# Optimization experiments

Hardware: AMD Instinct MI355X
Metric: run time of the kernel (lower is better)

Reference implementation:

```python
import jax, jax.numpy as jnp
import numpy as np

B, T, D, H = 2, 2048, 1024, 16
DK = D // H
SCALE = 1.0 / float(np.sqrt(DK))


def setup_inputs() -> dict:
    key0 = jax.random.key(0)
    ks = jax.random.split(key0, 12)
    std = 0.02
    inp = {
        "query": jax.random.normal(ks[0], (B, T, D), jnp.float32),
        "key": jax.random.normal(ks[1], (B, T, D), jnp.float32),
        "value": jax.random.normal(ks[2], (B, T, D), jnp.float32),
        # weights stored torch-style: out = x @ W.T + b, W is [D, D]
        "Wq": jax.random.normal(ks[3], (D, D), jnp.float32) * std,
        "bq": jnp.zeros((D,), jnp.float32),
        "Wk": jax.random.normal(ks[4], (D, D), jnp.float32) * std,
        "bk": jnp.zeros((D,), jnp.float32),
        "Wv": jax.random.normal(ks[5], (D, D), jnp.float32) * std,
        "bv": jnp.zeros((D,), jnp.float32),
        "Wo": jax.random.normal(ks[6], (D, D), jnp.float32) * std,
        "bo": jnp.zeros((D,), jnp.float32),
        # causal mask: True = masked out (matches masked_fill semantics)
        "attn_mask": jnp.triu(jnp.ones((T, T), jnp.bool_), k=1),
        # no padding (all False) to keep every softmax row valid
        "key_padding_mask": jnp.zeros((B, T), jnp.bool_),
    }
    return inp


def reference(query, key, value, Wq, bq, Wk, bk, Wv, bv, Wo, bo,
              attn_mask, key_padding_mask):
    Bq, Tq, _ = query.shape
    Tk = key.shape[1]
    # QKV projections, split into heads: [B, T, H, DK]
    q = (query @ Wq.T + bq).reshape(Bq, Tq, H, DK)
    k = (key @ Wk.T + bk).reshape(Bq, Tk, H, DK)
    v = (value @ Wv.T + bv).reshape(Bq, Tk, H, DK)
    # scaled dot-product scores: [B, H, Tq, Tk]
    scores = jnp.einsum("bqhd,bkhd->bhqk", q, k) * jnp.float32(SCALE)
    neg_inf = jnp.float32(-jnp.inf)
    scores = jnp.where(attn_mask[None, None, :, :], neg_inf, scores)
    scores = jnp.where(key_padding_mask[:, None, None, :], neg_inf, scores)
    attn = jax.nn.softmax(scores, axis=-1)
    out = jnp.einsum("bhqk,bkhd->bqhd", attn, v).reshape(Bq, Tq, D)
    return out @ Wo.T + bo
```

## Files before the change

### kernel.cpp

```cpp
#include <hip/hip_runtime.h>
#include <hip/hip_bf16.h>
#include <stdint.h>

#define B_   2
#define T_   2048
#define D_   1024
#define H_   16
#define DK_  64
#define KL2_ 0.18033688f

typedef __attribute__((ext_vector_type(8))) short   short8;
typedef __attribute__((ext_vector_type(4))) float   floatx4;
typedef unsigned short ushort_t;
typedef unsigned int   uint_t;

__device__ __forceinline__ ushort_t f32_to_bf16(float f) {
    union { float f; unsigned int u; } v; v.f = f;
    unsigned int r = v.u + 0x7fffu + ((v.u >> 16) & 1u);
    return (ushort_t)(r >> 16);
}

__device__ __forceinline__ uint_t pk_bf16(float lo, float hi) {
    uint_t ulo = __builtin_bit_cast(uint_t, lo) + 0x8000u;
    uint_t uhi = __builtin_bit_cast(uint_t, hi) + 0x8000u;
    return __builtin_amdgcn_perm(uhi, ulo, 0x07060302);
}

__device__ __forceinline__ void async_copy16(const ushort_t* g, ushort_t* l) {
    typedef const unsigned int __attribute__((address_space(1)))* gp_t;
    typedef       unsigned int __attribute__((address_space(3)))* lp_t;
    __builtin_amdgcn_global_load_lds((gp_t)(uintptr_t)g, (lp_t)(uintptr_t)l, 16, 0, 0);
}

__global__ __launch_bounds__(256) void cast_all_kernel(
    const float* __restrict__ q, const float* __restrict__ k, const float* __restrict__ v,
    const float* __restrict__ wq, const float* __restrict__ wk,
    const float* __restrict__ wv, const float* __restrict__ wo,
    ushort_t* __restrict__ oq, ushort_t* __restrict__ ok, ushort_t* __restrict__ ov,
    ushort_t* __restrict__ owq, ushort_t* __restrict__ owk,
    ushort_t* __restrict__ owv, ushort_t* __restrict__ owo)
{
    const int NTD4 = (B_ * T_ * D_) / 4;
    const int NW4  = (D_ * D_) / 4;
    int i = blockIdx.x * 256 + threadIdx.x;
    const float* s; ushort_t* d; int off;
    if (i < NTD4)              { s = q; d = oq; off = i; }
    else if (i < 2 * NTD4)     { s = k; d = ok; off = i - NTD4; }
    else if (i < 3 * NTD4)     { s = v; d = ov; off = i - 2 * NTD4; }
    else {
        int w = i - 3 * NTD4;
        int seg = w / NW4;  off = w - seg * NW4;
        s = (seg == 0) ? wq : (seg == 1) ? wk : (seg == 2) ? wv : wo;
        d = (seg == 0) ? owq : (seg == 1) ? owk : (seg == 2) ? owv : owo;
    }
    float4 x = ((const float4*)s)[off];
    ushort4 o;
    o.x = f32_to_bf16(x.x); o.y = f32_to_bf16(x.y);
    o.z = f32_to_bf16(x.z); o.w = f32_to_bf16(x.w);
    ((ushort4*)d)[off] = o;
}

#define BM 128
#define BK 32

template<int MODE, int NI>
__device__ __forceinline__ void gemm_bt_device(
    const ushort_t* __restrict__ A, const ushort_t* __restrict__ W,
    const float* __restrict__ bias, void* __restrict__ outp,
    int m0, int n0, ushort_t* sm, float oscale)
{
    const int tid  = threadIdx.x;
    const int lane = tid & 63;
    const int wv   = tid >> 6;
    const int wm   = (wv >> 1) * 64;
    const int wn   = (wv & 1) * (NI * 16);
    const int cl   = lane & 15;
    const int qd   = lane >> 4;
    const int sw4  = (cl >> 1) & 3;

    floatx4 acc[4][NI];
    const floatx4 z4 = {0.f, 0.f, 0.f, 0.f};
    #pragma unroll
    for (int mi = 0; mi < 4; ++mi)
        #pragma unroll
        for (int ni = 0; ni < NI; ++ni) acc[mi][ni] = z4;

    const int r0 = tid >> 2;
    const int cg = (tid & 3) ^ ((r0 >> 1) & 3);
    const ushort_t* Ag0 = A + (size_t)(m0 + r0) * 1024 + cg * 8;
    const ushort_t* Ag1 = A + (size_t)(m0 + 64 + r0) * 1024 + cg * 8;
    const ushort_t* Wg0 = W + (size_t)(n0 + r0) * 1024 + cg * 8;
    const ushort_t* Wg1 = W + (size_t)(n0 + 64 + r0) * 1024 + cg * 8;
    ushort_t* As0 = sm + tid * 8;
    ushort_t* As1 = sm + 2048 + tid * 8;
    ushort_t* Bs0 = sm + 4096 + tid * 8;
    ushort_t* Bs1 = sm + 6144 + tid * 8;

    for (int k0 = 0; k0 < 1024; k0 += BK) {
        async_copy16(Ag0 + k0, As0);
        async_copy16(Ag1 + k0, As1);
        async_copy16(Wg0 + k0, Bs0);
        if (NI == 4) async_copy16(Wg1 + k0, Bs1);
        __syncthreads();

        short8 af[4], bfr[NI];
        #pragma unroll
        for (int mi = 0; mi < 4; ++mi)
            af[mi] = *(const short8*)(sm + (wm + mi * 16 + cl) * 32 + (qd ^ sw4) * 8);
        #pragma unroll
        for (int ni = 0; ni < NI; ++ni)
            bfr[ni] = *(const short8*)(sm + 4096 + (wn + ni * 16 + cl) * 32 + (qd ^ sw4) * 8);

        #pragma unroll
        for (int mi = 0; mi < 4; ++mi)
            #pragma unroll
            for (int ni = 0; ni < NI; ++ni)
                acc[mi][ni] = __builtin_amdgcn_mfma_f32_16x16x32_bf16(
                    af[mi], bfr[ni], acc[mi][ni], 0, 0, 0);
        __syncthreads();
    }

    #pragma unroll
    for (int mi = 0; mi < 4; ++mi) {
        #pragma unroll
        for (int ni = 0; ni < NI; ++ni) {
            const int n = n0 + wn + ni * 16 + cl;
            const float bn = bias[n];
            if (MODE == 0) {
                float* out = (float*)outp;
                #pragma unroll
                for (int r = 0; r < 4; ++r) {
                    const int m = m0 + wm + mi * 16 + qd * 4 + r;
                    out[(size_t)m * D_ + n] = acc[mi][ni][r] + bn;
                }
            } else if (MODE == 1) {
                ushort_t* out = (ushort_t*)outp;
                const int h = n >> 6, dk = n & 63;
                #pragma unroll
                for (int r = 0; r < 4; ++r) {
                    const int m = m0 + wm + mi * 16 + qd * 4 + r;
                    const int b = m >> 11, t = m & (T_ - 1);
                    out[(((size_t)(b * H_ + h)) * T_ + t) * DK_ + dk] =
                        f32_to_bf16((acc[mi][ni][r] + bn) * oscale);
                }
            } else {
                ushort_t* out = (ushort_t*)outp;
                const int h = n >> 6, dk = n & 63;
                const int mb = m0 + wm + mi * 16 + qd * 4;
                const int b = mb >> 11, t0 = mb & (T_ - 1);
                const int tsw = (t0 & ~60) | ((t0 & 48) >> 2) | ((t0 & 12) << 2);
                ushort4 o;
                o.x = f32_to_bf16(acc[mi][ni][0] + bn);
                o.y = f32_to_bf16(acc[mi][ni][1] + bn);
                o.z = f32_to_bf16(acc[mi][ni][2] + bn);
                o.w = f32_to_bf16(acc[mi][ni][3] + bn);
                *(ushort4*)(out + (((size_t)(b * H_ + h)) * DK_ + dk) * T_ + tsw) = o;
            }
        }
    }
}

__global__ __launch_bounds__(256) void gemm_o_kernel(
    const ushort_t* __restrict__ A, const ushort_t* __restrict__ W,
    const float* __restrict__ bias, float* __restrict__ out)
{
    __shared__ __align__(16) ushort_t sm[8192];
    gemm_bt_device<0, 2>(A, W, bias, out, blockIdx.x * BM, blockIdx.y * 64, sm, 1.0f);
}


__device__ __forceinline__ void ldA4(short8 (&af)[4][2], const ushort_t* base, int coff) {
    #pragma unroll
    for (int mi = 0; mi < 4; ++mi) {
        af[mi][0] = *(const short8*)(base + mi * 1024 + coff);
        af[mi][1] = *(const short8*)(base + mi * 1024 + (coff ^ 32));
    }
}
__device__ __forceinline__ void ldB2(short8 (&bf)[2][2], const ushort_t* base, int coff) {
    #pragma unroll
    for (int ni = 0; ni < 2; ++ni) {
        bf[ni][0] = *(const short8*)(base + ni * 1024 + coff);
        bf[ni][1] = *(const short8*)(base + ni * 1024 + (coff ^ 32));
    }
}

template<int MQ, int NQ>
__device__ __forceinline__ void quad16(floatx4 (&acc)[8][4],
                                       const short8 (&af)[4][2],
                                       const short8 (&bf)[2][2])
{
    __builtin_amdgcn_s_setprio(1);
    #pragma unroll
    for (int mi = 0; mi < 4; ++mi)
        #pragma unroll
        for (int ni = 0; ni < 2; ++ni) {
            acc[MQ * 4 + mi][NQ * 2 + ni] = __builtin_amdgcn_mfma_f32_16x16x32_bf16(
                af[mi][0], bf[ni][0], acc[MQ * 4 + mi][NQ * 2 + ni], 0, 0, 0);
            acc[MQ * 4 + mi][NQ * 2 + ni] = __builtin_amdgcn_mfma_f32_16x16x32_bf16(
                af[mi][1], bf[ni][1], acc[MQ * 4 + mi][NQ * 2 + ni], 0, 0, 0);
        }
    __builtin_amdgcn_s_setprio(0);
}

__global__ void __launch_bounds__(512, 2) gemm_qkv8_kernel(
    const ushort_t* __restrict__ Xq, const ushort_t* __restrict__ Xk, const ushort_t* __restrict__ Xv,
    const ushort_t* __restrict__ Wqw, const ushort_t* __restrict__ Wkw, const ushort_t* __restrict__ Wvw,
    const float* __restrict__ bq, const float* __restrict__ bk, const float* __restrict__ bv,
    ushort_t* __restrict__ Qo, ushort_t* __restrict__ Ko, ushort_t* __restrict__ Vto)
{
    extern __shared__ __align__(16) ushort_t sm[];

    const int bid    = blockIdx.x;
    const int gid    = (bid & 7) * 24 + (bid >> 3);
    const int m_tile = gid / 12;
    const int n_tile = gid - m_tile * 12;
    const int m0     = m_tile * 256;
    const int seg    = n_tile >> 2;
    const int n0     = (n_tile & 3) * 256;

    const ushort_t* A    = (seg == 0) ? Xq  : (seg == 1) ? Xk  : Xv;
    const ushort_t* W    = (seg == 0) ? Wqw : (seg == 1) ? Wkw : Wvw;
    const float*    bias = (seg == 0) ? bq  : (seg == 1) ? bk  : bv;

    const int tid  = threadIdx.x;
    const int lane = tid & 63;
    const int wv   = tid >> 6;
    const int wm   = wv >> 2;
    const int wn   = wv & 3;
    const int cl   = lane & 15;
    const int qd   = lane >> 4;
    const int swz  = cl & 7;
    const int coff = (qd ^ swz) * 8;

    const int r0 = tid >> 3;
    const int c0 = (tid & 7) ^ (r0 & 7);
    const ushort_t* gA = A + (size_t)(m0 + r0) * 1024 + c0 * 8;
    const ushort_t* gB = W + (size_t)(n0 + r0) * 1024 + c0 * 8;
    ushort_t* lbase = sm + tid * 8;

    auto stage = [&](int t, int op, int h) {
        if (t >= 16) return;
        const ushort_t* g = (op ? gB : gA) + (size_t)h * 131072 + (size_t)t * 64;
        ushort_t* l = lbase + (size_t)((t & 1) * 4 + op * 2 + h) * 8192;
        async_copy16(g, l);
        async_copy16(g + 65536, l + 4096);
    };

    const ushort_t* A0 = sm + (0 * 4 + 0 * 2 + wm) * 8192 + cl * 64;
    const ushort_t* A1 = A0 + 4 * 8192;
    const ushort_t* B0 = sm + (0 * 4 + 1 * 2 + (wn >> 1)) * 8192 + (wn & 1) * 4096 + cl * 64;
    const ushort_t* B1 = B0 + 4 * 8192;

    floatx4 acc[8][4];
    const floatx4 z4 = {0.f, 0.f, 0.f, 0.f};
    #pragma unroll
    for (int i = 0; i < 8; ++i)
        #pragma unroll
        for (int j = 0; j < 4; ++j) acc[i][j] = z4;

    stage(0, 0, 0); stage(0, 0, 1); stage(0, 1, 0); stage(0, 1, 1);
    stage(1, 1, 0); stage(1, 1, 1);
    asm volatile("s_waitcnt vmcnt(4)" ::: "memory");
    __builtin_amdgcn_s_barrier();

    short8 af[4][2], bf0[2][2], bf1[2][2];

    #pragma unroll 1
    for (int it = 0; it < 7; ++it) {
        const int u = 2 * it, v = u + 1;
        ldA4(af, A0, coff); ldB2(bf0, B0, coff);
        stage(v, 0, 0);
        __builtin_amdgcn_s_barrier();
        quad16<0, 0>(acc, af, bf0);
        __builtin_amdgcn_s_barrier();
        ldB2(bf1, B0 + 2048, coff);
        stage(v, 0, 1);
        __builtin_amdgcn_s_barrier();
        quad16<0, 1>(acc, af, bf1);
        __builtin_amdgcn_s_barrier();
        ldA4(af, A0 + 4096, coff);
        stage(u + 2, 1, 0);
        __builtin_amdgcn_s_barrier();
        quad16<1, 1>(acc, af, bf1);
        __builtin_amdgcn_s_barrier();
        stage(u + 2, 1, 1);
        asm volatile("s_waitcnt vmcnt(4)" ::: "memory");
        __builtin_amdgcn_s_barrier();
        quad16<1, 0>(acc, af, bf0);
        __builtin_amdgcn_s_barrier();
        ldA4(af, A1, coff); ldB2(bf0, B1, coff);
        stage(u + 2, 0, 0);
        __builtin_amdgcn_s_barrier();
        quad16<0, 0>(acc, af, bf0);
        __builtin_amdgcn_s_barrier();
        ldB2(bf1, B1 + 2048, coff);
        stage(u + 2, 0, 1);
        __builtin_amdgcn_s_barrier();
        quad16<0, 1>(acc, af, bf1);
        __builtin_amdgcn_s_barrier();
        ldA4(af, A1 + 4096, coff);
        stage(v + 2, 1, 0);
        __builtin_amdgcn_s_barrier();
        quad16<1, 1>(acc, af, bf1);
        __builtin_amdgcn_s_barrier();
        stage(v + 2, 1, 1);
        asm volatile("s_waitcnt vmcnt(4)" ::: "memory");
        __builtin_amdgcn_s_barrier();
        quad16<1, 0>(acc, af, bf0);
        __builtin_amdgcn_s_barrier();
    }

    ldA4(af, A0, coff); ldB2(bf0, B0, coff);
    stage(15, 0, 0);
    __builtin_amdgcn_s_barrier();
    quad16<0, 0>(acc, af, bf0);
    __builtin_amdgcn_s_barrier();
    ldB2(bf1, B0 + 2048, coff);
    stage(15, 0, 1);
    __builtin_amdgcn_s_barrier();
    quad16<0, 1>(acc, af, bf1);
    __builtin_amdgcn_s_barrier();
    ldA4(af, A0 + 4096, coff);
    __builtin_amdgcn_s_barrier();
    quad16<1, 1>(acc, af, bf1);
    __builtin_amdgcn_s_barrier();
    asm volatile("s_waitcnt vmcnt(0)" ::: "memory");
    __builtin_amdgcn_s_barrier();
    quad16<1, 0>(acc, af, bf0);
    __builtin_amdgcn_s_barrier();
    ldA4(af, A1, coff); ldB2(bf0, B1, coff);
    __builtin_amdgcn_s_barrier();
    quad16<0, 0>(acc, af, bf0);
    __builtin_amdgcn_s_barrier();
    ldB2(bf1, B1 + 2048, coff);
    __builtin_amdgcn_s_barrier();
    quad16<0, 1>(acc, af, bf1);
    __builtin_amdgcn_s_barrier();
    ldA4(af, A1 + 4096, coff);
    __builtin_amdgcn_s_barrier();
    quad16<1, 1>(acc, af, bf1);
    __builtin_amdgcn_s_barrier();
    quad16<1, 0>(acc, af, bf0);

    float bn[4];
    #pragma unroll
    for (int nf = 0; nf < 4; ++nf)
        bn[nf] = bias[n0 + wn * 64 + nf * 16 + cl];

    if (seg < 2) {
        ushort_t* out = (seg == 0) ? Qo : Ko;
        const float oscale = (seg == 0) ? KL2_ : 1.0f;
        #pragma unroll
        for (int mf = 0; mf < 8; ++mf) {
            #pragma unroll
            for (int nf = 0; nf < 4; ++nf) {
                const int n = n0 + wn * 64 + nf * 16 + cl;
                const int h = n >> 6, dk = n & 63;
                #pragma unroll
                for (int r = 0; r < 4; ++r) {
                    const int m = m0 + wm * 128 + mf * 16 + qd * 4 + r;
                    const int b = m >> 11, t = m & (T_ - 1);
                    out[(((size_t)(b * H_ + h)) * T_ + t) * DK_ + dk] =
                        f32_to_bf16((acc[mf][nf][r] + bn[nf]) * oscale);
                }
            }
        }
    } else {
        #pragma unroll
        for (int mf = 0; mf < 8; ++mf) {
            #pragma unroll
            for (int nf = 0; nf < 4; ++nf) {
                const int n = n0 + wn * 64 + nf * 16 + cl;
                const int h = n >> 6, dk = n & 63;
                const int mb = m0 + wm * 128 + mf * 16 + qd * 4;
                const int b = mb >> 11, t0 = mb & (T_ - 1);
                const int tsw = (t0 & ~60) | ((t0 & 48) >> 2) | ((t0 & 12) << 2);
                ushort4 o;
                o.x = f32_to_bf16(acc[mf][nf][0] + bn[nf]);
                o.y = f32_to_bf16(acc[mf][nf][1] + bn[nf]);
                o.z = f32_to_bf16(acc[mf][nf][2] + bn[nf]);
                o.w = f32_to_bf16(acc[mf][nf][3] + bn[nf]);
                *(ushort4*)(Vto + (((size_t)(b * H_ + h)) * DK_ + dk) * T_ + tsw) = o;
            }
        }
    }
}

__global__ __launch_bounds__(256, 2) void attn_kernel(
    const ushort_t* __restrict__ Q, const ushort_t* __restrict__ K,
    const ushort_t* __restrict__ Vs, ushort_t* __restrict__ O)
{
    __shared__ __align__(16) ushort_t sm[32768];
    const int tid  = threadIdx.x;
    const int lane = tid & 63;
    const int wv   = tid >> 6;
    const int cl   = lane & 15;
    const int qd   = lane >> 4;
    const int swz  = cl & 7;
    const int h = blockIdx.x & (H_ - 1), b = blockIdx.x >> 4;
    const int p   = blockIdx.y;
    const int btA = 31 - p;

    const ushort_t* Qh = Q  + ((size_t)(b * H_ + h) * T_) * DK_;
    const ushort_t* Kh = K  + ((size_t)(b * H_ + h) * T_) * DK_;
    const ushort_t* Vh = Vs + ((size_t)(b * H_ + h) * DK_) * T_;

    const int sr  = tid >> 3;
    const int sc  = tid & 7;
    const int scg = sc ^ (sr & 7);

    auto stage_step = [&](int s) {
        const int kbase = ((s <= btA) ? s : (s - btA - 1)) << 6;
        ushort_t* Kb = sm + (s & 3) * 8192;
        ushort_t* Vb = Kb + 4096;
        #pragma unroll
        for (int rr = 0; rr < 2; ++rr) {
            const int r = rr * 32 + sr;
            async_copy16(Kh + (size_t)(kbase + r) * DK_ + scg * 8, Kb + r * 64 + sc * 8);
            async_copy16(Vh + (size_t)r * T_ + kbase + scg * 8,    Vb + r * 64 + sc * 8);
        }
    };

    int qw = btA * 64 + wv * 16;
    short8 qf0 = *(const short8*)(Qh + (size_t)(qw + cl) * DK_ + qd * 8);
    short8 qf1 = *(const short8*)(Qh + (size_t)(qw + cl) * DK_ + 32 + qd * 8);

    stage_step(0);
    stage_step(1);

    const floatx4 z4 = {0.f, 0.f, 0.f, 0.f};
    floatx4 oaccT[4] = {z4, z4, z4, z4};
    float l_ = 0.f;

    auto flush = [&](int q0w) {
        float l = l_;
        l += __shfl_xor(l, 16, 64);
        l += __shfl_xor(l, 32, 64);
        const float inv = 1.0f / l;
        ushort_t* Ob = O + ((size_t)(b * T_ + q0w + cl)) * D_ + h * DK_ + qd * 4;
        #pragma unroll
        for (int dt = 0; dt < 4; ++dt) {
            ushort4 o;
            o.x = f32_to_bf16(oaccT[dt][0] * inv);
            o.y = f32_to_bf16(oaccT[dt][1] * inv);
            o.z = f32_to_bf16(oaccT[dt][2] * inv);
            o.w = f32_to_bf16(oaccT[dt][3] * inv);
            *(ushort4*)(Ob + dt * 16) = o;
        }
    };

    auto compute_step = [&](int s) {
        const bool inA  = (s <= btA);
        const int kbase = (inA ? s : (s - btA - 1)) << 6;
        const bool diag = inA ? (s == btA) : (s == 32);
        ushort_t* cb = sm + (s & 3) * 8192;
        short8 kb[4][2];
        #pragma unroll
        for (int m = 0; m < 4; ++m)
            #pragma unroll
            for (int i = 0; i < 2; ++i)
                kb[m][i] = *(const short8*)(cb + (m * 16 + cl) * 64 + ((i * 4 + qd) ^ swz) * 8);
        floatx4 sacc[4] = {z4, z4, z4, z4};
        #pragma unroll
        for (int i = 0; i < 2; ++i)
            #pragma unroll
            for (int m = 0; m < 4; ++m)
                sacc[m] = __builtin_amdgcn_mfma_f32_16x16x32_bf16(
                    kb[m][i], (i ? qf1 : qf0), sacc[m], 0, 0, 0);
        const int qabs = qw + cl;
        float pr[4][4];
        if (diag) {
            #pragma unroll
            for (int c = 0; c < 4; ++c)
                #pragma unroll
                for (int r = 0; r < 4; ++r) {
                    const bool keep = (kbase + c * 16 + qd * 4 + r) <= qabs;
                    const float e = __builtin_amdgcn_exp2f(sacc[c][r]);
                    pr[c][r] = keep ? e : 0.f;
                    l_ += pr[c][r];
                }
        } else {
            #pragma unroll
            for (int c = 0; c < 4; ++c)
                #pragma unroll
                for (int r = 0; r < 4; ++r) {
                    pr[c][r] = __builtin_amdgcn_exp2f(sacc[c][r]);
                    l_ += pr[c][r];
                }
        }
        short8 va2[4][2];
        #pragma unroll
        for (int dt = 0; dt < 4; ++dt)
            #pragma unroll
            for (int h2 = 0; h2 < 2; ++h2)
                va2[dt][h2] = *(const short8*)(cb + 4096 + (dt * 16 + cl) * 64 +
                                               ((qd * 2 + h2) ^ swz) * 8);
        #pragma unroll
        for (int cp = 0; cp < 2; ++cp) {
            union { uint_t u[4]; short8 v; } pb;
            pb.u[0] = pk_bf16(pr[cp * 2][0],     pr[cp * 2][1]);
            pb.u[1] = pk_bf16(pr[cp * 2][2],     pr[cp * 2][3]);
            pb.u[2] = pk_bf16(pr[cp * 2 + 1][0], pr[cp * 2 + 1][1]);
            pb.u[3] = pk_bf16(pr[cp * 2 + 1][2], pr[cp * 2 + 1][3]);
            #pragma unroll
            for (int dt = 0; dt < 4; ++dt)
                oaccT[dt] = __builtin_amdgcn_mfma_f32_16x16x32_bf16(
                    va2[dt][cp], pb.v, oaccT[dt], 0, 0, 0);
        }
        if (s == btA) {
            flush(qw);
            #pragma unroll
            for (int dt = 0; dt < 4; ++dt) oaccT[dt] = z4;
            l_ = 0.f;
            qw = p * 64 + wv * 16;
            qf0 = *(const short8*)(Qh + (size_t)(qw + cl) * DK_ + qd * 8);
            qf1 = *(const short8*)(Qh + (size_t)(qw + cl) * DK_ + 32 + qd * 8);
        }
    };

    for (int g = 0; g < 17; ++g) {
        const int s0 = g * 2;
        __syncthreads();
        if (s0 + 2 <= 32) stage_step(s0 + 2);
        if (s0 + 3 <= 32) stage_step(s0 + 3);
        compute_step(s0);
        if (s0 + 1 <= 32) compute_step(s0 + 1);
    }
    flush(qw);
}

extern "C" void kernel_launch(void* const* d_in, const int* in_sizes, int n_in,
                              void* d_out, int out_size, void* d_ws, size_t ws_size,
                              hipStream_t stream)
{
    const float* q_in = (const float*)d_in[0];
    const float* k_in = (const float*)d_in[1];
    const float* v_in = (const float*)d_in[2];
    const float* Wq   = (const float*)d_in[3];
    const float* bq   = (const float*)d_in[4];
    const float* Wk   = (const float*)d_in[5];
    const float* bk   = (const float*)d_in[6];
    const float* Wv   = (const float*)d_in[7];
    const float* bv   = (const float*)d_in[8];
    const float* Wo   = (const float*)d_in[9];
    const float* bo   = (const float*)d_in[10];
    float* out = (float*)d_out;

    const size_t NTD = (size_t)B_ * T_ * D_;
    const size_t NW  = (size_t)D_ * D_;
    ushort_t* ws  = (ushort_t*)d_ws;
    ushort_t* Xq  = ws;
    ushort_t* Xk  = Xq + NTD;
    ushort_t* Xv  = Xk + NTD;
    ushort_t* Wqb = Xv + NTD;
    ushort_t* Wkb = Wqb + NW;
    ushort_t* Wvb = Wkb + NW;
    ushort_t* Wob = Wvb + NW;
    ushort_t* Qd  = Wob + NW;
    ushort_t* Kd  = Qd + NTD;
    ushort_t* Vtd = Kd + NTD;
    ushort_t* Od  = Vtd + NTD;

    const int total4 = (int)((3 * NTD + 4 * NW) / 4);
    cast_all_kernel<<<dim3(total4 / 256), dim3(256), 0, stream>>>(
        q_in, k_in, v_in, Wq, Wk, Wv, Wo,
        Xq, Xk, Xv, Wqb, Wkb, Wvb, Wob);

    static bool s_attr = false;
    if (!s_attr) {
        (void)hipFuncSetAttribute((const void*)gemm_qkv8_kernel,
                                  hipFuncAttributeMaxDynamicSharedMemorySize, 131072);
        s_attr = true;
    }
    gemm_qkv8_kernel<<<dim3(192), dim3(512), 131072, stream>>>(
        Xq, Xk, Xv, Wqb, Wkb, Wvb, bq, bk, bv, Qd, Kd, Vtd);

    attn_kernel<<<dim3(32, 16), dim3(256), 0, stream>>>(Qd, Kd, Vtd, Od);

    gemm_o_kernel<<<dim3(32, 16), dim3(256), 0, stream>>>(Od, Wob, bo, out);
}
```

Measured before the change: 211.6 us.

## Double-buffer output projection GEMM with wider K tiles and async prefetch

The output-projection GEMM is rewritten as a standalone kernel that uses a K tile of 64 instead of 32 and double-buffers the shared-memory tiles. The next tile's async copies are issued before computing on the current one, and there is one barrier per iteration instead of two. The aim is to hide global-load latency and halve synchronization overhead. In exchange, shared memory per block grows threefold and launch bounds now request two blocks per CU, which may pressure occupancy or registers.

Result: no change. 210.2 us (-0.7%).

```diff
diff --git a/kernel.cpp b/kernel.cpp
--- a/kernel.cpp
+++ b/kernel.cpp
@@ -60,114 +60,93 @@
     ((ushort4*)d)[off] = o;
 }
 
-#define BM 128
-#define BK 32
-
-template<int MODE, int NI>
-__device__ __forceinline__ void gemm_bt_device(
+__global__ __launch_bounds__(256, 2) void gemm_o_kernel(
     const ushort_t* __restrict__ A, const ushort_t* __restrict__ W,
-    const float* __restrict__ bias, void* __restrict__ outp,
-    int m0, int n0, ushort_t* sm, float oscale)
+    const float* __restrict__ bias, float* __restrict__ out)
 {
+    __shared__ __align__(16) ushort_t sm[24576];
     const int tid  = threadIdx.x;
     const int lane = tid & 63;
     const int wv   = tid >> 6;
     const int wm   = (wv >> 1) * 64;
-    const int wn   = (wv & 1) * (NI * 16);
+    const int wn   = (wv & 1) * 32;
     const int cl   = lane & 15;
     const int qd   = lane >> 4;
-    const int sw4  = (cl >> 1) & 3;
-
-    floatx4 acc[4][NI];
+    const int swz  = cl & 7;
+    const int coff = (qd ^ swz) * 8;
+    const int m0 = blockIdx.x * 128, n0 = blockIdx.y * 64;
+
+    const int r0 = tid >> 3;
+    const int c0 = (tid & 7) ^ (r0 & 7);
+    const ushort_t* Ag = A + (size_t)(m0 + r0) * 1024 + c0 * 8;
+    const ushort_t* Wg = W + (size_t)(n0 + r0) * 1024 + c0 * 8;
+    const int ldst = r0 * 64 + (tid & 7) * 8;
+
+    auto stage = [&](int t, int buf) {
+        const ushort_t* ga = Ag + t * 64;
+        const ushort_t* gb = Wg + t * 64;
+        ushort_t* la = sm + buf * 12288 + ldst;
+        ushort_t* lb = sm + buf * 12288 + 8192 + ldst;
+        async_copy16(ga,             la);
+        async_copy16(ga + 32 * 1024, la + 32 * 64);
+        async_copy16(ga + 64 * 1024, la + 64 * 64);
+        async_copy16(ga + 96 * 1024, la + 96 * 64);
+        async_copy16(gb,             lb);
+        async_copy16(gb + 32 * 1024, lb + 32 * 64);
+    };
+
+    floatx4 acc[4][2];
     const floatx4 z4 = {0.f, 0.f, 0.f, 0.f};
     #pragma unroll
-    for (int mi = 0; mi < 4; ++mi)
-        #pragma unroll
-        for (int ni = 0; ni < NI; ++ni) acc[mi][ni] = z4;
-
-    const int r0 = tid >> 2;
-    const int cg = (tid & 3) ^ ((r0 >> 1) & 3);
-    const ushort_t* Ag0 = A + (size_t)(m0 + r0) * 1024 + cg * 8;
-    const ushort_t* Ag1 = A + (size_t)(m0 + 64 + r0) * 1024 + cg * 8;
-    const ushort_t* Wg0 = W + (size_t)(n0 + r0) * 1024 + cg * 8;
-    const ushort_t* Wg1 = W + (size_t)(n0 + 64 + r0) * 1024 + cg * 8;
-    ushort_t* As0 = sm + tid * 8;
-    ushort_t* As1 = sm + 2048 + tid * 8;
-    ushort_t* Bs0 = sm + 4096 + tid * 8;
-    ushort_t* Bs1 = sm + 6144 + tid * 8;
-
-    for (int k0 = 0; k0 < 1024; k0 += BK) {
-        async_copy16(Ag0 + k0, As0);
-        async_copy16(Ag1 + k0, As1);
-        async_copy16(Wg0 + k0, Bs0);
-        if (NI == 4) async_copy16(Wg1 + k0, Bs1);
+    for (int mi = 0; mi < 4; ++mi) { acc[mi][0] = z4; acc[mi][1] = z4; }
+
+    stage(0, 0);
+    __syncthreads();
+
+    #pragma unroll 1
+    for (int t = 0; t < 16; ++t) {
+        const int cur = t & 1;
+        if (t < 15) stage(t + 1, cur ^ 1);
+
+        const ushort_t* Ab = sm + cur * 12288 + (wm + cl) * 64;
+        const ushort_t* Bb = sm + cur * 12288 + 8192 + (wn + cl) * 64;
+        short8 af[4][2], bf[2][2];
+        #pragma unroll
+        for (int mi = 0; mi < 4; ++mi) {
+            af[mi][0] = *(const short8*)(Ab + mi * 1024 + coff);
+            af[mi][1] = *(const short8*)(Ab + mi * 1024 + (coff ^ 32));
+        }
+        #pragma unroll
+        for (int ni = 0; ni < 2; ++ni) {
+            bf[ni][0] = *(const short8*)(Bb + ni * 1024 + coff);
+            bf[ni][1] = *(const short8*)(Bb + ni * 1024 + (coff ^ 32));
+        }
+        #pragma unroll
+        for (int mi = 0; mi < 4; ++mi)
+            #pragma unroll
+            for (int ni = 0; ni < 2; ++ni) {
+                acc[mi][ni] = __builtin_amdgcn_mfma_f32_16x16x32_bf16(
+                    af[mi][0], bf[ni][0], acc[mi][ni], 0, 0, 0);
+                acc[mi][ni] = __builtin_amdgcn_mfma_f32_16x16x32_bf16(
+                    af[mi][1], bf[ni][1], acc[mi][ni], 0, 0, 0);
+            }
         __syncthreads();
-
-        short8 af[4], bfr[NI];
-        #pragma unroll
-        for (int mi = 0; mi < 4; ++mi)
-            af[mi] = *(const short8*)(sm + (wm + mi * 16 + cl) * 32 + (qd ^ sw4) * 8);
-        #pragma unroll
-        for (int ni = 0; ni < NI; ++ni)
-            bfr[ni] = *(const short8*)(sm + 4096 + (wn + ni * 16 + cl) * 32 + (qd ^ sw4) * 8);
-
-        #pragma unroll
-        for (int mi = 0; mi < 4; ++mi)
-            #pragma unroll
-            for (int ni = 0; ni < NI; ++ni)
-                acc[mi][ni] = __builtin_amdgcn_mfma_f32_16x16x32_bf16(
-                    af[mi], bfr[ni], acc[mi][ni], 0, 0, 0);
-        __syncthreads();
     }
 
     #pragma unroll
     for (int mi = 0; mi < 4; ++mi) {
         #pragma unroll
-        for (int ni = 0; ni < NI; ++ni) {
+        for (int ni = 0; ni < 2; ++ni) {
             const int n = n0 + wn + ni * 16 + cl;
             const float bn = bias[n];
-            if (MODE == 0) {
-                float* out = (float*)outp;
-                #pragma unroll
-                for (int r = 0; r < 4; ++r) {
-                    const int m = m0 + wm + mi * 16 + qd * 4 + r;
-                    out[(size_t)m * D_ + n] = acc[mi][ni][r] + bn;
-                }
-            } else if (MODE == 1) {
-                ushort_t* out = (ushort_t*)outp;
-                const int h = n >> 6, dk = n & 63;
-                #pragma unroll
-                for (int r = 0; r < 4; ++r) {
-                    const int m = m0 + wm + mi * 16 + qd * 4 + r;
-                    const int b = m >> 11, t = m & (T_ - 1);
-                    out[(((size_t)(b * H_ + h)) * T_ + t) * DK_ + dk] =
-                        f32_to_bf16((acc[mi][ni][r] + bn) * oscale);
-                }
-            } else {
-                ushort_t* out = (ushort_t*)outp;
-                const int h = n >> 6, dk = n & 63;
-                const int mb = m0 + wm + mi * 16 + qd * 4;
-                const int b = mb >> 11, t0 = mb & (T_ - 1);
-                const int tsw = (t0 & ~60) | ((t0 & 48) >> 2) | ((t0 & 12) << 2);
-                ushort4 o;
-                o.x = f32_to_bf16(acc[mi][ni][0] + bn);
-                o.y = f32_to_bf16(acc[mi][ni][1] + bn);
-                o.z = f32_to_bf16(acc[mi][ni][2] + bn);
-                o.w = f32_to_bf16(acc[mi][ni][3] + bn);
-                *(ushort4*)(out + (((size_t)(b * H_ + h)) * DK_ + dk) * T_ + tsw) = o;
+            #pragma unroll
+            for (int r = 0; r < 4; ++r) {
+                const int m = m0 + wm + mi * 16 + qd * 4 + r;
+                out[(size_t)m * D_ + n] = acc[mi][ni][r] + bn;
             }
         }
     }
 }
-
-__global__ __launch_bounds__(256) void gemm_o_kernel(
-    const ushort_t* __restrict__ A, const ushort_t* __restrict__ W,
-    const float* __restrict__ bias, float* __restrict__ out)
-{
-    __shared__ __align__(16) ushort_t sm[8192];
-    gemm_bt_device<0, 2>(A, W, bias, out, blockIdx.x * BM, blockIdx.y * 64, sm, 1.0f);
-}
-
 
 __device__ __forceinline__ void ldA4(short8 (&af)[4][2], const ushort_t* base, int coff) {
     #pragma unroll
```
